# Optimization experiments

Hardware: AMD Instinct MI355X
Metric: run time of the kernel (lower is better)

Reference implementation:

```python
import jax, jax.numpy as jnp
import numpy as np

MODEL_DIM = 1024
EXPAND = 2
INNER = MODEL_DIM * EXPAND      # 2048
STATE = 16
K = 4                           # conv kernel
B, S = 2, 1024


def setup_inputs() -> dict:
    key = jax.random.key(0)
    ks = jax.random.split(key, 12)
    sd = 0.02
    hidden = jax.random.normal(ks[0], (B, S, MODEL_DIM), dtype=jnp.float32)
    w_in = jax.random.normal(ks[1], (2 * INNER, MODEL_DIM), dtype=jnp.float32) * sd
    w_conv = jax.random.normal(ks[2], (INNER, 1, K), dtype=jnp.float32) * 0.2   # depthwise [O, I/g=1, K]
    b_conv = jax.random.normal(ks[3], (INNER,), dtype=jnp.float32) * 0.02
    w_dt = jax.random.normal(ks[4], (INNER, INNER), dtype=jnp.float32) * sd
    b_dt = jnp.full((INNER,), -2.0, dtype=jnp.float32)  # small softplus(dt) at init
    w_b = jax.random.normal(ks[5], (INNER * STATE, INNER), dtype=jnp.float32) * sd
    w_c = jax.random.normal(ks[6], (INNER * STATE, INNER), dtype=jnp.float32) * sd
    w_out = jax.random.normal(ks[7], (MODEL_DIM, INNER), dtype=jnp.float32) * sd
    # a_log = log(arange(1, N+1)) repeated over inner_dim
    a_log = jnp.log(jnp.tile(jnp.arange(1, STATE + 1, dtype=jnp.float32), (INNER, 1)))
    d = jnp.ones((INNER,), dtype=jnp.float32)
    return {"hidden": hidden, "w_in": w_in, "w_conv": w_conv, "b_conv": b_conv,
            "w_dt": w_dt, "b_dt": b_dt, "w_b": w_b, "w_c": w_c, "w_out": w_out,
            "a_log": a_log, "d": d}


def reference(hidden, w_in, w_conv, b_conv, w_dt, b_dt, w_b, w_c, w_out, a_log, d):
    batch, seq_len, _ = hidden.shape
    inner, state_n = a_log.shape
    k = w_conv.shape[-1]

    proj = hidden @ w_in.T                     # [B,S,2*inner]
    u, gate = jnp.split(proj, 2, axis=-1)

    # depthwise causal conv: torch pads k-1 both sides then slices [:, :, :S]
    # which equals left-only padding of k-1
    x = u.transpose(0, 2, 1)                   # [B,inner,S]
    x = jax.lax.conv_general_dilated(
        x, w_conv, window_strides=(1,), padding=[(k - 1, 0)],
        dimension_numbers=("NCH", "OIH", "NCH"), feature_group_count=inner)
    u = jax.nn.silu(x.transpose(0, 2, 1) + b_conv)   # [B,S,inner]
    gate = jax.nn.sigmoid(gate)

    delta = jax.nn.softplus(u @ w_dt.T + b_dt)                       # [B,S,inner]
    bmat = (u @ w_b.T).reshape(batch, seq_len, inner, state_n)       # [B,S,inner,N]
    cmat = (u @ w_c.T).reshape(batch, seq_len, inner, state_n)
    a = -jnp.exp(a_log)                                              # [inner,N]

    def step(state, xs):
        d_t, u_t, b_t, c_t, g_t = xs
        state = jnp.exp(d_t[..., None] * a) * state + d_t[..., None] * b_t * u_t[..., None]
        y = jnp.sum(c_t * state, axis=-1) + d * u_t
        return state, y * g_t

    xs = (delta.transpose(1, 0, 2), u.transpose(1, 0, 2),
          bmat.transpose(1, 0, 2, 3), cmat.transpose(1, 0, 2, 3),
          gate.transpose(1, 0, 2))
    init = jnp.zeros((batch, inner, state_n), dtype=hidden.dtype)
    _, ys = jax.lax.scan(step, init, xs)       # ys: [S,B,inner]
    mixed = ys.transpose(1, 0, 2)              # [B,S,inner]
    return mixed @ w_out.T                     # dropout is identity in eval mode
```

## Files before the change

kernel.cpp:

```cpp
#include <hip/hip_runtime.h>
#include <hip/hip_bf16.h>

typedef __bf16 bf16_t;
typedef __bf16 bf16x8 __attribute__((ext_vector_type(8)));
typedef float f32x4 __attribute__((ext_vector_type(4)));

#define MODEL_DIM 1024
#define INNER 2048
#define STATE 16
#define BATCH 2
#define SEQ 1024
#define BS (BATCH * SEQ)
#define PROJ_N (2 * INNER)
#define BCN (INNER * STATE)
#define NCHUNK 64
#define CLEN (SEQ / NCHUNK)

__device__ __forceinline__ void load_lds_16B(const void* g, void* l) {
  __builtin_amdgcn_global_load_lds(
      (const __attribute__((address_space(1))) unsigned int*)g,
      (__attribute__((address_space(3))) unsigned int*)l,
      16, 0, 0);
}

__global__ void cast_f32_bf16(const float* __restrict__ in,
                              bf16_t* __restrict__ out, long n4) {
  long idx = (long)blockIdx.x * blockDim.x + threadIdx.x;
  long stride = (long)gridDim.x * blockDim.x;
  for (long i = idx; i < n4; i += stride) {
    float4 v = ((const float4*)in)[i];
    union { bf16_t b[4]; ushort4 u; } cv;
    cv.b[0] = (bf16_t)v.x; cv.b[1] = (bf16_t)v.y;
    cv.b[2] = (bf16_t)v.z; cv.b[3] = (bf16_t)v.w;
    ((ushort4*)out)[i] = cv.u;
  }
}

__global__ __launch_bounds__(512, 2)
void gemm_big8(const bf16_t* __restrict__ Ap, const bf16_t* __restrict__ Bp,
               bf16_t* __restrict__ C, int N, int K) {
  __shared__ bf16_t As[2 * 256 * 64];
  __shared__ bf16_t Bs[2 * 256 * 64];
  const int tid = threadIdx.x;
  const int wid = tid >> 6, lane = tid & 63;
  const int wm = wid >> 2, wn = wid & 3;

  const int bid = blockIdx.x;
  const int xcd = bid & 7, local = bid >> 3;
  const int bcol = (xcd * 16 + (local >> 3)) * 256;
  const int brow = (local & 7) * 256;

  const int lrow = lane >> 3;
  const int l7 = lane & 7;
  const int scol = (l7 ^ lrow) * 8;
  const int r15 = lane & 15, g = lane >> 4;

  const int NT = K >> 6, NI = NT >> 1;

  f32x4 acc[8][4] = {};
  bf16x8 af[4][2], vb0[2][2], vb1[2][2];

#define FENCE() asm volatile("" ::: "memory")
#define VM_WAIT(n) asm volatile("s_waitcnt vmcnt(" #n ")" ::: "memory")

#define STAGE_A(BUF, T, H)                                                    \
  {                                                                           \
    _Pragma("unroll") for (int j = 0; j < 2; ++j) {                           \
      const int rs = j * 128 + (H) * 64;                                      \
      load_lds_16B(Ap + (size_t)(brow + rs + wid * 8 + lrow) * K +            \
                       (size_t)(T) * 64 + scol,                               \
                   (void*)(As + (BUF) * 16384 + rs * 64 + wid * 512));        \
    }                                                                         \
  }
#define STAGE_B(BUF, T, H)                                                    \
  {                                                                           \
    _Pragma("unroll") for (int j = 0; j < 2; ++j) {                           \
      const int rs = (2 * j + (wid >> 2)) * 64 + (H) * 32 + (wid & 3) * 8;    \
      load_lds_16B(Bp + (size_t)(bcol + rs + lrow) * K +                      \
                       (size_t)(T) * 64 + scol,                               \
                   (void*)(Bs + (BUF) * 16384 + rs * 64));                    \
    }                                                                         \
  }

#define LOAD_A(BUF, MH)                                                       \
  _Pragma("unroll") for (int m = 0; m < 4; ++m) {                             \
    int arow = wm * 128 + (MH) * 64 + m * 16 + r15;                           \
    _Pragma("unroll") for (int ks = 0; ks < 2; ++ks)                          \
      af[m][ks] = *(const bf16x8*)&As[(BUF) * 16384 + arow * 64 +             \
                                      (((ks * 4 + g) ^ l7) * 8)];             \
  }
#define LOAD_B(BUF, NH, DST)                                                  \
  _Pragma("unroll") for (int n = 0; n < 2; ++n) {                             \
    int brw = wn * 64 + (NH) * 32 + n * 16 + r15;                             \
    _Pragma("unroll") for (int ks = 0; ks < 2; ++ks)                          \
      DST[n][ks] = *(const bf16x8*)&Bs[(BUF) * 16384 + brw * 64 +             \
                                       (((ks * 4 + g) ^ l7) * 8)];            \
  }

#define PHASE(MH, NH, BSEL, LOADS, STAGE_CODE, WAITC)                         \
  {                                                                           \
    LOADS;                                                                    \
    STAGE_CODE;                                                               \
    FENCE();                                                                  \
    __builtin_amdgcn_s_setprio(1);                                            \
    _Pragma("unroll") for (int ks = 0; ks < 2; ++ks)                          \
      _Pragma("unroll") for (int m = 0; m < 4; ++m)                           \
        _Pragma("unroll") for (int n = 0; n < 2; ++n)                         \
          acc[(MH) * 4 + m][(NH) * 2 + n] =                                   \
              __builtin_amdgcn_mfma_f32_16x16x32_bf16(                        \
                  af[m][ks], BSEL[n][ks], acc[(MH) * 4 + m][(NH) * 2 + n],    \
                  0, 0, 0);                                                   \
    __builtin_amdgcn_s_setprio(0);                                            \
    WAITC;                                                                    \
    FENCE();                                                                  \
    __builtin_amdgcn_s_barrier();                                             \
    FENCE();                                                                  \
  }

  STAGE_A(0, 0, 0); STAGE_A(0, 0, 1); STAGE_B(0, 0, 0); STAGE_B(0, 0, 1);
  STAGE_A(1, 1, 0); STAGE_B(1, 1, 0);
  VM_WAIT(4);
  __builtin_amdgcn_s_barrier();
  FENCE();

  for (int i = 0; i < NI - 1; ++i) {
    const int t1 = 2 * i + 1, t2 = 2 * i + 2, t3 = 2 * i + 3;
    PHASE(0, 0, vb0, {LOAD_A(0, 0); LOAD_B(0, 0, vb0);}, STAGE_B(1, t1, 1), );
    PHASE(0, 1, vb1, LOAD_B(0, 1, vb1),                  STAGE_A(1, t1, 1), );
    PHASE(1, 0, vb0, LOAD_A(0, 1),                       STAGE_A(0, t2, 0), );
    PHASE(1, 1, vb1, ,                                   STAGE_B(0, t2, 0), VM_WAIT(4));
    PHASE(0, 0, vb0, {LOAD_A(1, 0); LOAD_B(1, 0, vb0);}, STAGE_B(0, t2, 1), );
    PHASE(0, 1, vb1, LOAD_B(1, 1, vb1),                  STAGE_A(0, t2, 1), );
    PHASE(1, 0, vb0, LOAD_A(1, 1),                       STAGE_A(1, t3, 0), );
    PHASE(1, 1, vb1, ,                                   STAGE_B(1, t3, 0), VM_WAIT(4));
  }
  {
    const int tl = NT - 1;
    PHASE(0, 0, vb0, {LOAD_A(0, 0); LOAD_B(0, 0, vb0);}, STAGE_B(1, tl, 1), );
    PHASE(0, 1, vb1, LOAD_B(0, 1, vb1),                  STAGE_A(1, tl, 1), );
    PHASE(1, 0, vb0, LOAD_A(0, 1),                       , );
    PHASE(1, 1, vb1, ,                                   , VM_WAIT(2));
    PHASE(0, 0, vb0, {LOAD_A(1, 0); LOAD_B(1, 0, vb0);}, , VM_WAIT(0));
    PHASE(0, 1, vb1, LOAD_B(1, 1, vb1),                  , );
    PHASE(1, 0, vb0, LOAD_A(1, 1),                       , );
    PHASE(1, 1, vb1, ,                                   , );
  }
#undef PHASE
#undef LOAD_A
#undef LOAD_B
#undef STAGE_A
#undef STAGE_B
#undef VM_WAIT
#undef FENCE

#pragma unroll
  for (int mf = 0; mf < 8; ++mf) {
#pragma unroll
    for (int nf = 0; nf < 4; ++nf) {
      int col = bcol + wn * 64 + nf * 16 + r15;
#pragma unroll
      for (int j = 0; j < 4; ++j) {
        int row = brow + wm * 128 + mf * 16 + g * 4 + j;
        C[(size_t)row * N + col] = (bf16_t)acc[mf][nf][j];
      }
    }
  }
}

template <int EPI>
__global__ __launch_bounds__(256)
void gemm_bt(const bf16_t* __restrict__ A, const bf16_t* __restrict__ Bt,
             void* __restrict__ C, const float* __restrict__ bias,
             int nbx, int nby, int N, int K) {
  __shared__ bf16_t Ash[128 * 64];
  __shared__ bf16_t Bsh[128 * 64];
  const int tid = threadIdx.x;
  const int wave = tid >> 6, lane = tid & 63;

  const int bid = blockIdx.x;
  const int xcd = bid & 7, local = bid >> 3;
  const int bcol = (xcd * (nbx >> 3) + local / nby) * 128;
  const int brow = (local % nby) * 128;

  const int wr = wave >> 1, wc = wave & 1;

  f32x4 acc[4][4] = {};

  const int seg_base = wave * 4;
  const int lrow = lane >> 3;
  const int scol = ((lane & 7) ^ (lrow & 7)) * 8;
  const int r15 = lane & 15, g = lane >> 4, l7 = lane & 7;

  for (int k0 = 0; k0 < K; k0 += 64) {
#pragma unroll
    for (int c = 0; c < 4; ++c) {
      int seg = seg_base + c;
      int row = seg * 8 + lrow;
      const bf16_t* ga = A + (size_t)(brow + row) * K + k0 + scol;
      load_lds_16B(ga, (void*)(Ash + seg * 512));
      const bf16_t* gb = Bt + (size_t)(bcol + row) * K + k0 + scol;
      load_lds_16B(gb, (void*)(Bsh + seg * 512));
    }
    asm volatile("s_waitcnt vmcnt(0)");
    __syncthreads();

#pragma unroll
    for (int ks = 0; ks < 2; ++ks) {
      bf16x8 af[4], bfr[4];
#pragma unroll
      for (int t = 0; t < 4; ++t) {
        int arow = wr * 64 + t * 16 + r15;
        int brw  = wc * 64 + t * 16 + r15;
        int slot = ((ks * 4 + g) ^ l7) * 8;
        af[t]  = *(const bf16x8*)&Ash[arow * 64 + slot];
        bfr[t] = *(const bf16x8*)&Bsh[brw * 64 + slot];
      }
#pragma unroll
      for (int mt = 0; mt < 4; ++mt)
#pragma unroll
        for (int nt = 0; nt < 4; ++nt)
          acc[mt][nt] = __builtin_amdgcn_mfma_f32_16x16x32_bf16(
              af[mt], bfr[nt], acc[mt][nt], 0, 0, 0);
    }
    __syncthreads();
  }

#pragma unroll
  for (int mt = 0; mt < 4; ++mt) {
#pragma unroll
    for (int nt = 0; nt < 4; ++nt) {
      int col = bcol + wc * 64 + nt * 16 + r15;
#pragma unroll
      for (int j = 0; j < 4; ++j) {
        int row = brow + wr * 64 + mt * 16 + g * 4 + j;
        float v = acc[mt][nt][j];
        size_t idx = (size_t)row * N + col;
        if (EPI == 0) {
          ((float*)C)[idx] = v;
        } else if (EPI == 1) {
          float x = v + bias[col];
          ((float*)C)[idx] = (x > 20.f) ? x : log1pf(__expf(x));
        } else {
          ((bf16_t*)C)[idx] = (bf16_t)v;
        }
      }
    }
  }
}

__global__ __launch_bounds__(256)
void conv_silu(const float* __restrict__ proj, const float* __restrict__ w_conv,
               const float* __restrict__ b_conv, bf16_t* __restrict__ u_bf,
               bf16_t* __restrict__ gate_bf) {
  int idx = blockIdx.x * 256 + threadIdx.x;
  int i = idx & (INNER - 1);
  int s = (idx >> 11) & (SEQ - 1);
  int b = idx >> 21;
  const float* up = proj + (size_t)b * SEQ * PROJ_N + i;
  float w0 = w_conv[i * 4 + 0], w1 = w_conv[i * 4 + 1];
  float w2 = w_conv[i * 4 + 2], w3 = w_conv[i * 4 + 3];
  float acc = b_conv[i];
  acc += up[(size_t)s * PROJ_N] * w3;
  if (s >= 1) acc += up[(size_t)(s - 1) * PROJ_N] * w2;
  if (s >= 2) acc += up[(size_t)(s - 2) * PROJ_N] * w1;
  if (s >= 3) acc += up[(size_t)(s - 3) * PROJ_N] * w0;
  float u = acc / (1.f + __expf(-acc));
  u_bf[idx] = (bf16_t)u;
  float gp = up[(size_t)s * PROJ_N + INNER];
  gate_bf[idx] = (bf16_t)(1.f / (1.f + __expf(-gp)));
}

__global__ __launch_bounds__(256)
void scan_pass1(const float* __restrict__ delta, const bf16_t* __restrict__ u,
                const bf16_t* __restrict__ bmat, const float* __restrict__ a_log,
                float* __restrict__ P, float* __restrict__ E) {
  int t = blockIdx.x * 256 + threadIdx.x;
  int i = t & (INNER - 1);
  int c = (t >> 11) & (NCHUNK - 1);
  int b = t >> 17;
  float an[STATE];
#pragma unroll
  for (int n = 0; n < STATE; ++n) an[n] = -__expf(a_log[i * STATE + n]);
  float st[STATE] = {};
  float dtsum = 0.f;
  size_t base_ch = (size_t)b * SEQ * INNER + i;
  size_t base_bc = (size_t)b * SEQ * BCN + (size_t)i * STATE;
  int s0 = c * CLEN;
  for (int s = s0; s < s0 + CLEN; ++s) {
    float dt = delta[base_ch + (size_t)s * INNER];
    float uv = (float)u[base_ch + (size_t)s * INNER];
    bf16x8 b0 = *(const bf16x8*)&bmat[base_bc + (size_t)s * BCN];
    bf16x8 b1 = *(const bf16x8*)&bmat[base_bc + (size_t)s * BCN + 8];
    float du = dt * uv;
    dtsum += dt;
#pragma unroll
    for (int n = 0; n < 8; ++n)
      st[n] = __expf(dt * an[n]) * st[n] + du * (float)b0[n];
#pragma unroll
    for (int n = 0; n < 8; ++n)
      st[8 + n] = __expf(dt * an[8 + n]) * st[8 + n] + du * (float)b1[n];
  }
  size_t pe = ((size_t)(b * NCHUNK + c) * INNER + i) * STATE;
#pragma unroll
  for (int q = 0; q < 4; ++q) {
    f32x4 vp = {__expf(dtsum * an[q * 4]), __expf(dtsum * an[q * 4 + 1]),
                __expf(dtsum * an[q * 4 + 2]), __expf(dtsum * an[q * 4 + 3])};
    *(f32x4*)&P[pe + q * 4] = vp;
    f32x4 ve = {st[q * 4], st[q * 4 + 1], st[q * 4 + 2], st[q * 4 + 3]};
    *(f32x4*)&E[pe + q * 4] = ve;
  }
}

__global__ __launch_bounds__(256)
void scan_mid(const float* __restrict__ P, float* __restrict__ E) {
  int gi = blockIdx.x * 256 + threadIdx.x;
  int n = gi & (STATE - 1);
  int i = (gi >> 4) & (INNER - 1);
  int b = gi >> 15;
  float H = 0.f;
  size_t stride = (size_t)INNER * STATE;
  size_t idx = (size_t)b * NCHUNK * stride + (size_t)i * STATE + n;
  for (int c = 0; c < NCHUNK; ++c) {
    float p = P[idx];
    float e = E[idx];
    E[idx] = H;
    H = p * H + e;
    idx += stride;
  }
}

__global__ __launch_bounds__(256)
void scan_pass2(const float* __restrict__ delta, const bf16_t* __restrict__ u,
                const bf16_t* __restrict__ bmat, const bf16_t* __restrict__ cmat,
                const bf16_t* __restrict__ gate, const float* __restrict__ a_log,
                const float* __restrict__ dvec, const float* __restrict__ E,
                bf16_t* __restrict__ mixed) {
  int t = blockIdx.x * 256 + threadIdx.x;
  int i = t & (INNER - 1);
  int c = (t >> 11) & (NCHUNK - 1);
  int b = t >> 17;
  float an[STATE];
#pragma unroll
  for (int n = 0; n < STATE; ++n) an[n] = -__expf(a_log[i * STATE + n]);
  float st[STATE];
  size_t pe = ((size_t)(b * NCHUNK + c) * INNER + i) * STATE;
#pragma unroll
  for (int q = 0; q < 4; ++q) {
    f32x4 v = *(const f32x4*)&E[pe + q * 4];
    st[q * 4] = v[0]; st[q * 4 + 1] = v[1]; st[q * 4 + 2] = v[2]; st[q * 4 + 3] = v[3];
  }
  float dd = dvec[i];
  size_t base_ch = (size_t)b * SEQ * INNER + i;
  size_t base_bc = (size_t)b * SEQ * BCN + (size_t)i * STATE;
  int s0 = c * CLEN;
  for (int s = s0; s < s0 + CLEN; ++s) {
    float dt = delta[base_ch + (size_t)s * INNER];
    float uv = (float)u[base_ch + (size_t)s * INNER];
    bf16x8 b0 = *(const bf16x8*)&bmat[base_bc + (size_t)s * BCN];
    bf16x8 b1 = *(const bf16x8*)&bmat[base_bc + (size_t)s * BCN + 8];
    bf16x8 c0 = *(const bf16x8*)&cmat[base_bc + (size_t)s * BCN];
    bf16x8 c1 = *(const bf16x8*)&cmat[base_bc + (size_t)s * BCN + 8];
    float du = dt * uv;
    float y = 0.f;
#pragma unroll
    for (int n = 0; n < 8; ++n) {
      st[n] = __expf(dt * an[n]) * st[n] + du * (float)b0[n];
      y += (float)c0[n] * st[n];
    }
#pragma unroll
    for (int n = 0; n < 8; ++n) {
      st[8 + n] = __expf(dt * an[8 + n]) * st[8 + n] + du * (float)b1[n];
      y += (float)c1[n] * st[8 + n];
    }
    float g = (float)gate[base_ch + (size_t)s * INNER];
    mixed[base_ch + (size_t)s * INNER] = (bf16_t)((y + dd * uv) * g);
  }
}

extern "C" void kernel_launch(void* const* d_in, const int* in_sizes, int n_in,
                              void* d_out, int out_size, void* d_ws, size_t ws_size,
                              hipStream_t stream) {
  const float* hidden = (const float*)d_in[0];
  const float* w_in   = (const float*)d_in[1];
  const float* w_conv = (const float*)d_in[2];
  const float* b_conv = (const float*)d_in[3];
  const float* w_dt   = (const float*)d_in[4];
  const float* b_dt   = (const float*)d_in[5];
  const float* w_b    = (const float*)d_in[6];
  const float* w_c    = (const float*)d_in[7];
  const float* w_out  = (const float*)d_in[8];
  const float* a_log  = (const float*)d_in[9];
  const float* dvec   = (const float*)d_in[10];
  float* out = (float*)d_out;

  char* ws = (char*)d_ws;
  bf16_t* hidden_bf = (bf16_t*)ws; ws += (size_t)BS * MODEL_DIM * 2;
  bf16_t* wsmall_bf = (bf16_t*)ws; ws += (size_t)PROJ_N * MODEL_DIM * 2;
  float*  proj      = (float*)ws;  ws += (size_t)BS * PROJ_N * 4;
  bf16_t* u_bf      = (bf16_t*)ws; ws += (size_t)BS * INNER * 2;
  bf16_t* gate_bf   = (bf16_t*)ws; ws += (size_t)BS * INNER * 2;
  float*  delta     = (float*)ws;  ws += (size_t)BS * INNER * 4;
  bf16_t* wbig_bf   = (bf16_t*)ws; ws += (size_t)BCN * INNER * 2;
  bf16_t* bmat      = (bf16_t*)ws; ws += (size_t)BS * BCN * 2;
  bf16_t* cmat      = (bf16_t*)ws; ws += (size_t)BS * BCN * 2;
  bf16_t* mixed     = (bf16_t*)ws; ws += (size_t)BS * INNER * 2;
  float* Pbuf = (float*)wbig_bf;
  float* Ebuf = Pbuf + (size_t)BATCH * NCHUNK * INNER * STATE;

  cast_f32_bf16<<<2048, 256, 0, stream>>>(hidden, hidden_bf, (long)BS * MODEL_DIM / 4);
  cast_f32_bf16<<<2048, 256, 0, stream>>>(w_in, wsmall_bf, (long)PROJ_N * MODEL_DIM / 4);
  gemm_bt<0><<<32 * 16, 256, 0, stream>>>(
      hidden_bf, wsmall_bf, proj, nullptr, 32, 16, PROJ_N, MODEL_DIM);
  conv_silu<<<(BATCH * SEQ * INNER) / 256, 256, 0, stream>>>(proj, w_conv, b_conv, u_bf, gate_bf);
  cast_f32_bf16<<<2048, 256, 0, stream>>>(w_dt, wsmall_bf, (long)INNER * INNER / 4);
  gemm_bt<1><<<16 * 16, 256, 0, stream>>>(
      u_bf, wsmall_bf, delta, b_dt, 16, 16, INNER, INNER);
  cast_f32_bf16<<<2048, 256, 0, stream>>>(w_b, wbig_bf, (long)BCN * INNER / 4);
  gemm_big8<<<1024, 512, 0, stream>>>(u_bf, wbig_bf, bmat, BCN, INNER);
  cast_f32_bf16<<<2048, 256, 0, stream>>>(w_c, wbig_bf, (long)BCN * INNER / 4);
  gemm_big8<<<1024, 512, 0, stream>>>(u_bf, wbig_bf, cmat, BCN, INNER);
  scan_pass1<<<(BATCH * NCHUNK * INNER) / 256, 256, 0, stream>>>(
      delta, u_bf, bmat, a_log, Pbuf, Ebuf);
  scan_mid<<<(BATCH * INNER * STATE) / 256, 256, 0, stream>>>(Pbuf, Ebuf);
  scan_pass2<<<(BATCH * NCHUNK * INNER) / 256, 256, 0, stream>>>(
      delta, u_bf, bmat, cmat, gate_bf, a_log, dvec, Ebuf, mixed);
  cast_f32_bf16<<<2048, 256, 0, stream>>>(w_out, wsmall_bf, (long)MODEL_DIM * INNER / 4);
  gemm_bt<0><<<8 * 16, 256, 0, stream>>>(
      mixed, wsmall_bf, out, nullptr, 8, 16, MODEL_DIM, INNER);
}
```

Before: 1.009 ms.

## Fuse fp32-to-bf16 weight cast into big B/C projection GEMM loader

The big w_b/w_c GEMMs now read the fp32 weights directly, staging them through registers and converting them to bf16 before the LDS write. This drops two separate cast kernels and the write and re-read of a 128 MB bf16 weight copy each. In exchange the GEMM reads fp32 weights, twice the bytes of the old bf16 path, and replaces the async global-to-LDS loads with register staging and lgkm waits, which could hurt overlap. The scan buffers now get their own workspace instead of aliasing the weight buffer.

```diff
diff --git a/kernel.cpp b/kernel.cpp
--- a/kernel.cpp
+++ b/kernel.cpp
@@ -37,7 +37,7 @@
 }
 
 __global__ __launch_bounds__(512, 2)
-void gemm_big8(const bf16_t* __restrict__ Ap, const bf16_t* __restrict__ Bp,
+void gemm_big8(const bf16_t* __restrict__ Ap, const float* __restrict__ Bp,
                bf16_t* __restrict__ C, int N, int K) {
   __shared__ bf16_t As[2 * 256 * 64];
   __shared__ bf16_t Bs[2 * 256 * 64];
@@ -59,9 +59,11 @@
 
   f32x4 acc[8][4] = {};
   bf16x8 af[4][2], vb0[2][2], vb1[2][2];
+  f32x4 bA[2][2], bB[2][2], bC[2][2];
 
 #define FENCE() asm volatile("" ::: "memory")
 #define VM_WAIT(n) asm volatile("s_waitcnt vmcnt(" #n ")" ::: "memory")
+#define LGKM0 asm volatile("s_waitcnt lgkmcnt(0)" ::: "memory")
 
 #define STAGE_A(BUF, T, H)                                                    \
   {                                                                           \
@@ -72,13 +74,26 @@
                    (void*)(As + (BUF) * 16384 + rs * 64 + wid * 512));        \
     }                                                                         \
   }
-#define STAGE_B(BUF, T, H)                                                    \
+#define BLOAD(SLOT, T, H)                                                     \
   {                                                                           \
     _Pragma("unroll") for (int j = 0; j < 2; ++j) {                           \
       const int rs = (2 * j + (wid >> 2)) * 64 + (H) * 32 + (wid & 3) * 8;    \
-      load_lds_16B(Bp + (size_t)(bcol + rs + lrow) * K +                      \
-                       (size_t)(T) * 64 + scol,                               \
-                   (void*)(Bs + (BUF) * 16384 + rs * 64));                    \
+      const float* gsrc = Bp + (size_t)(bcol + rs + lrow) * K +               \
+                          (size_t)(T) * 64 + ((l7 ^ lrow) * 8);               \
+      SLOT[j][0] = *(const f32x4*)gsrc;                                       \
+      SLOT[j][1] = *(const f32x4*)(gsrc + 4);                                 \
+    }                                                                         \
+  }
+#define BWRITE(SLOT, BUF, H)                                                  \
+  {                                                                           \
+    _Pragma("unroll") for (int j = 0; j < 2; ++j) {                           \
+      const int rs = (2 * j + (wid >> 2)) * 64 + (H) * 32 + (wid & 3) * 8;    \
+      union { bf16_t h[8]; bf16x8 v; } cv;                                    \
+      _Pragma("unroll") for (int e = 0; e < 4; ++e) {                         \
+        cv.h[e] = (bf16_t)SLOT[j][0][e];                                      \
+        cv.h[4 + e] = (bf16_t)SLOT[j][1][e];                                  \
+      }                                                                       \
+      *(bf16x8*)&Bs[(BUF) * 16384 + (rs + lrow) * 64 + l7 * 8] = cv.v;        \
     }                                                                         \
   }
 
@@ -117,40 +132,44 @@
     FENCE();                                                                  \
   }
 
-  STAGE_A(0, 0, 0); STAGE_A(0, 0, 1); STAGE_B(0, 0, 0); STAGE_B(0, 0, 1);
-  STAGE_A(1, 1, 0); STAGE_B(1, 1, 0);
-  VM_WAIT(4);
+  BLOAD(bA, 0, 0); BLOAD(bB, 0, 1); BLOAD(bC, 1, 0);
+  STAGE_A(0, 0, 0); STAGE_A(0, 0, 1); STAGE_A(1, 1, 0);
+  BWRITE(bA, 0, 0); BWRITE(bB, 0, 1);
+  LGKM0;
+  VM_WAIT(2);
   __builtin_amdgcn_s_barrier();
   FENCE();
 
   for (int i = 0; i < NI - 1; ++i) {
     const int t1 = 2 * i + 1, t2 = 2 * i + 2, t3 = 2 * i + 3;
-    PHASE(0, 0, vb0, {LOAD_A(0, 0); LOAD_B(0, 0, vb0);}, STAGE_B(1, t1, 1), );
-    PHASE(0, 1, vb1, LOAD_B(0, 1, vb1),                  STAGE_A(1, t1, 1), );
-    PHASE(1, 0, vb0, LOAD_A(0, 1),                       STAGE_A(0, t2, 0), );
-    PHASE(1, 1, vb1, ,                                   STAGE_B(0, t2, 0), VM_WAIT(4));
-    PHASE(0, 0, vb0, {LOAD_A(1, 0); LOAD_B(1, 0, vb0);}, STAGE_B(0, t2, 1), );
-    PHASE(0, 1, vb1, LOAD_B(1, 1, vb1),                  STAGE_A(0, t2, 1), );
-    PHASE(1, 0, vb0, LOAD_A(1, 1),                       STAGE_A(1, t3, 0), );
-    PHASE(1, 1, vb1, ,                                   STAGE_B(1, t3, 0), VM_WAIT(4));
+    PHASE(0, 0, vb0, {LOAD_A(0, 0); LOAD_B(0, 0, vb0);}, BLOAD(bA, t1, 1), );
+    PHASE(0, 1, vb1, LOAD_B(0, 1, vb1), {STAGE_A(1, t1, 1); BWRITE(bC, 1, 0);}, LGKM0);
+    PHASE(1, 0, vb0, LOAD_A(0, 1),      {STAGE_A(0, t2, 0); BWRITE(bA, 1, 1);}, LGKM0);
+    PHASE(1, 1, vb1, ,                   BLOAD(bA, t2, 0),                      VM_WAIT(4));
+    PHASE(0, 0, vb0, {LOAD_A(1, 0); LOAD_B(1, 0, vb0);}, BLOAD(bB, t2, 1), );
+    PHASE(0, 1, vb1, LOAD_B(1, 1, vb1), {STAGE_A(0, t2, 1); BWRITE(bA, 0, 0);}, LGKM0);
+    PHASE(1, 0, vb0, LOAD_A(1, 1),      {STAGE_A(1, t3, 0); BWRITE(bB, 0, 1);}, LGKM0);
+    PHASE(1, 1, vb1, ,                   BLOAD(bC, t3, 0),                      VM_WAIT(4));
   }
   {
     const int tl = NT - 1;
-    PHASE(0, 0, vb0, {LOAD_A(0, 0); LOAD_B(0, 0, vb0);}, STAGE_B(1, tl, 1), );
-    PHASE(0, 1, vb1, LOAD_B(0, 1, vb1),                  STAGE_A(1, tl, 1), );
-    PHASE(1, 0, vb0, LOAD_A(0, 1),                       , );
-    PHASE(1, 1, vb1, ,                                   , VM_WAIT(2));
-    PHASE(0, 0, vb0, {LOAD_A(1, 0); LOAD_B(1, 0, vb0);}, , VM_WAIT(0));
-    PHASE(0, 1, vb1, LOAD_B(1, 1, vb1),                  , );
-    PHASE(1, 0, vb0, LOAD_A(1, 1),                       , );
-    PHASE(1, 1, vb1, ,                                   , );
+    PHASE(0, 0, vb0, {LOAD_A(0, 0); LOAD_B(0, 0, vb0);}, BLOAD(bA, tl, 1), );
+    PHASE(0, 1, vb1, LOAD_B(0, 1, vb1), {STAGE_A(1, tl, 1); BWRITE(bC, 1, 0);}, LGKM0);
+    PHASE(1, 0, vb0, LOAD_A(0, 1),       BWRITE(bA, 1, 1),                      LGKM0);
+    PHASE(1, 1, vb1, ,                   ,                                      VM_WAIT(2));
+    PHASE(0, 0, vb0, {LOAD_A(1, 0); LOAD_B(1, 0, vb0);}, ,                      VM_WAIT(0));
+    PHASE(0, 1, vb1, LOAD_B(1, 1, vb1), , );
+    PHASE(1, 0, vb0, LOAD_A(1, 1),      , );
+    PHASE(1, 1, vb1, ,                  , );
   }
 #undef PHASE
 #undef LOAD_A
 #undef LOAD_B
 #undef STAGE_A
-#undef STAGE_B
+#undef BLOAD
+#undef BWRITE
 #undef VM_WAIT
+#undef LGKM0
 #undef FENCE
 
 #pragma unroll
@@ -400,12 +419,11 @@
   bf16_t* u_bf      = (bf16_t*)ws; ws += (size_t)BS * INNER * 2;
   bf16_t* gate_bf   = (bf16_t*)ws; ws += (size_t)BS * INNER * 2;
   float*  delta     = (float*)ws;  ws += (size_t)BS * INNER * 4;
-  bf16_t* wbig_bf   = (bf16_t*)ws; ws += (size_t)BCN * INNER * 2;
+  float*  Pbuf      = (float*)ws;  ws += (size_t)BATCH * NCHUNK * INNER * STATE * 4;
+  float*  Ebuf      = (float*)ws;  ws += (size_t)BATCH * NCHUNK * INNER * STATE * 4;
   bf16_t* bmat      = (bf16_t*)ws; ws += (size_t)BS * BCN * 2;
   bf16_t* cmat      = (bf16_t*)ws; ws += (size_t)BS * BCN * 2;
   bf16_t* mixed     = (bf16_t*)ws; ws += (size_t)BS * INNER * 2;
-  float* Pbuf = (float*)wbig_bf;
-  float* Ebuf = Pbuf + (size_t)BATCH * NCHUNK * INNER * STATE;
 
   cast_f32_bf16<<<2048, 256, 0, stream>>>(hidden, hidden_bf, (long)BS * MODEL_DIM / 4);
   cast_f32_bf16<<<2048, 256, 0, stream>>>(w_in, wsmall_bf, (long)PROJ_N * MODEL_DIM / 4);
@@ -415,10 +433,8 @@
   cast_f32_bf16<<<2048, 256, 0, stream>>>(w_dt, wsmall_bf, (long)INNER * INNER / 4);
   gemm_bt<1><<<16 * 16, 256, 0, stream>>>(
       u_bf, wsmall_bf, delta, b_dt, 16, 16, INNER, INNER);
-  cast_f32_bf16<<<2048, 256, 0, stream>>>(w_b, wbig_bf, (long)BCN * INNER / 4);
-  gemm_big8<<<1024, 512, 0, stream>>>(u_bf, wbig_bf, bmat, BCN, INNER);
-  cast_f32_bf16<<<2048, 256, 0, stream>>>(w_c, wbig_bf, (long)BCN * INNER / 4);
-  gemm_big8<<<1024, 512, 0, stream>>>(u_bf, wbig_bf, cmat, BCN, INNER);
+  gemm_big8<<<1024, 512, 0, stream>>>(u_bf, w_b, bmat, BCN, INNER);
+  gemm_big8<<<1024, 512, 0, stream>>>(u_bf, w_c, cmat, BCN, INNER);
   scan_pass1<<<(BATCH * NCHUNK * INNER) / 256, 256, 0, stream>>>(
       delta, u_bf, bmat, a_log, Pbuf, Ebuf);
   scan_mid<<<(BATCH * INNER * STATE) / 256, 256, 0, stream>>>(Pbuf, Ebuf);
```

After: 1.192 ms. 18.1% more time.
